# Kernel tuning notes

Hardware: AMD Instinct MI355X
Metric: run time of the kernel (lower is better)

## Reference

```python
import jax, jax.numpy as jnp
import numpy as np

EPS = 1e-5
ALPHA = 1.0

def _conv1x1(x, w, b):
    # x: [N,C,T,V], w: [O,C], b: [O] -> [N,O,T,V]
    return jnp.einsum('nctv,oc->notv', x, w) + b[None, :, None, None]

def _groupnorm1(x, gamma, beta):
    # GroupNorm(1, C): normalize over (C,T,V) per sample
    mu = jnp.mean(x, axis=(1, 2, 3), keepdims=True)
    var = jnp.var(x, axis=(1, 2, 3), keepdims=True)
    xn = (x - mu) * jax.lax.rsqrt(var + EPS)
    return xn * gamma[None, :, None, None] + beta[None, :, None, None]

def setup_inputs() -> dict:
    key = jax.random.key(0)
    ks = jax.random.split(key, 12)
    N, Cin, T, V, O, R = 128, 64, 128, 25, 64, 8
    s_in = 1.0 / np.sqrt(Cin)
    s_r = 1.0 / np.sqrt(R)
    return {
        'x':  jax.random.normal(ks[0], (N, Cin, T, V), jnp.float32),
        'A':  jax.random.normal(ks[1], (V, V), jnp.float32) * 0.1,
        'w1': jax.random.normal(ks[2], (R, Cin), jnp.float32) * s_in,
        'b1': jnp.zeros((R,), jnp.float32),
        'g1': jnp.ones((R,), jnp.float32),
        'be1': jnp.zeros((R,), jnp.float32),
        'w2': jax.random.normal(ks[3], (R, Cin), jnp.float32) * s_in,
        'b2': jnp.zeros((R,), jnp.float32),
        'g2': jnp.ones((R,), jnp.float32),
        'be2': jnp.zeros((R,), jnp.float32),
        'w3': jax.random.normal(ks[4], (O, Cin), jnp.float32) * s_in,
        'b3': jnp.zeros((O,), jnp.float32),
        'w4': jax.random.normal(ks[5], (O, R), jnp.float32) * s_r,
        'b4': jnp.zeros((O,), jnp.float32),
    }

def reference(x, A, w1, b1, g1, be1, w2, b2, g2, be2, w3, b3, w4, b4):
    # branch 1: conv1 -> GroupNorm -> temporal mean -> pairwise diff -> tanh
    x1 = _groupnorm1(_conv1x1(x, w1, b1), g1, be1).mean(axis=2)      # [N,R,V]
    y1 = jnp.tanh(x1[..., :, None] - x1[..., None, :])               # [N,R,V,V]
    # branch 2: conv2 -> GroupNorm -> temporal mean -> outer product -> tanh
    x2 = _groupnorm1(_conv1x1(x, w2, b2), g2, be2).mean(axis=2)      # [N,R,V]
    y2 = jnp.tanh(x2[..., :, None] * x2[..., None, :])               # [N,R,V,V]
    # value branch
    x3 = _conv1x1(x, w3, b3)                                          # [N,O,T,V]
    # dynamic adjacency: conv4 over rel channels
    ys = y1 + ALPHA * y2 + A[None, None]                              # [N,R,V,V]
    y_sum = jnp.einsum('nruv,or->nouv', ys, w4) + b4[None, :, None, None]
    # aggregation over vertices
    y = jnp.einsum('ncuv,nctv->nctu', y_sum, x3)                      # [N,O,T,V]
    return y
```

## Files before the change

### kernel.cpp

```cpp
#include <hip/hip_runtime.h>

#define EPSV 1e-5f
constexpr int NN = 128, CIN = 64, TT = 128, VV = 25, OO = 64, RR = 8;
constexpr int TVQ   = TT * VV;
constexpr int XSAMP = CIN * TVQ;
constexpr int YSAMP = OO * TT * VV;
constexpr int RTV   = RR * TT * VV;
constexpr int S12N  = 2 * RR * VV;
constexpr int YST_SAMP = VV * VV * OO;

__global__ __launch_bounds__(256) void kZero(float* __restrict__ p, int n)
{
    int i = blockIdx.x * 256 + threadIdx.x;
    if (i < n) p[i] = 0.f;
}

__global__ __launch_bounds__(256) void kA(const float* __restrict__ x,
    const float* __restrict__ w1, const float* __restrict__ b1,
    const float* __restrict__ w2, const float* __restrict__ b2,
    float* __restrict__ s12g, float* __restrict__ ssqg)
{
    __shared__ float wt1[CIN * RR], wt2[CIN * RR];
    __shared__ float s1l[RR * VV], s2l[RR * VV];
    __shared__ float redA[4], redB[4];
    const int tid = threadIdx.x;
    const int tc  = blockIdx.x;
    const int n   = blockIdx.y;

    for (int e = tid; e < CIN * RR; e += 256) {
        int r = e >> 6, c = e & 63;
        wt1[c * RR + r] = w1[e];
        wt2[c * RR + r] = w2[e];
    }
    for (int e = tid; e < 2 * RR * VV; e += 256) {
        if (e < RR * VV) s1l[e] = 0.f; else s2l[e - RR * VV] = 0.f;
    }
    __syncthreads();

    float acc1[4][RR], acc2[4][RR];
    #pragma unroll
    for (int j = 0; j < 4; ++j)
        #pragma unroll
        for (int r = 0; r < RR; ++r) { acc1[j][r] = 0.f; acc2[j][r] = 0.f; }

    const bool active = (tid < 200);
    const int p0 = tid * 4;
    const float* xb = x + (size_t)n * XSAMP + tc * 800 + p0;
    if (active) {
        #pragma unroll 4
        for (int c = 0; c < CIN; ++c) {
            float4 xv  = *(const float4*)(xb + c * TVQ);
            float4 wa1 = *(const float4*)(&wt1[c * RR]);
            float4 wb1 = *(const float4*)(&wt1[c * RR + 4]);
            float4 wa2 = *(const float4*)(&wt2[c * RR]);
            float4 wb2 = *(const float4*)(&wt2[c * RR + 4]);
            float xj[4]  = {xv.x, xv.y, xv.z, xv.w};
            float w1v[8] = {wa1.x, wa1.y, wa1.z, wa1.w, wb1.x, wb1.y, wb1.z, wb1.w};
            float w2v[8] = {wa2.x, wa2.y, wa2.z, wa2.w, wb2.x, wb2.y, wb2.z, wb2.w};
            #pragma unroll
            for (int j = 0; j < 4; ++j)
                #pragma unroll
                for (int r = 0; r < RR; ++r) {
                    acc1[j][r] += w1v[r] * xj[j];
                    acc2[j][r] += w2v[r] * xj[j];
                }
        }
    }

    float b1r[RR], b2r[RR];
    #pragma unroll
    for (int r = 0; r < RR; ++r) { b1r[r] = b1[r]; b2r[r] = b2[r]; }

    float ssq1 = 0.f, ssq2 = 0.f;
    if (active) {
        #pragma unroll
        for (int j = 0; j < 4; ++j) {
            int v = (p0 + j) % VV;
            #pragma unroll
            for (int r = 0; r < RR; ++r) {
                float c1 = acc1[j][r] + b1r[r]; ssq1 += c1 * c1;
                float c2 = acc2[j][r] + b2r[r]; ssq2 += c2 * c2;
                atomicAdd(&s1l[r * VV + v], acc1[j][r]);
                atomicAdd(&s2l[r * VV + v], acc2[j][r]);
            }
        }
    }
    #pragma unroll
    for (int off = 32; off > 0; off >>= 1) {
        ssq1 += __shfl_down(ssq1, off);
        ssq2 += __shfl_down(ssq2, off);
    }
    if ((tid & 63) == 0) { redA[tid >> 6] = ssq1; redB[tid >> 6] = ssq2; }
    __syncthreads();
    for (int e = tid; e < S12N; e += 256) {
        float pv = (e < RR * VV) ? s1l[e] : s2l[e - RR * VV];
        atomicAdd(&s12g[n * S12N + e], pv);
    }
    if (tid == 0) {
        atomicAdd(&ssqg[n * 2 + 0], redA[0] + redA[1] + redA[2] + redA[3]);
        atomicAdd(&ssqg[n * 2 + 1], redB[0] + redB[1] + redB[2] + redB[3]);
    }
}

__device__ __forceinline__ float tanh_fast(float v)
{
    float e = __expf(2.f * v);
    return 1.f - 2.f / (e + 1.f);
}

__global__ __launch_bounds__(512) void kB(
    const float* __restrict__ s12g, const float* __restrict__ ssqg,
    const float* __restrict__ b1, const float* __restrict__ g1, const float* __restrict__ be1,
    const float* __restrict__ b2, const float* __restrict__ g2, const float* __restrict__ be2,
    const float* __restrict__ Amat, const float* __restrict__ w4, const float* __restrict__ b4,
    float* __restrict__ ysumT)
{
    __shared__ float x1g[RR * VV], x2g[RR * VV];
    __shared__ float w4l[OO * RR];
    __shared__ float b4l[OO];
    __shared__ float stats[2];
    __shared__ float mss[4];
    const int tid = threadIdx.x;
    const int bx  = blockIdx.x;
    const int n   = blockIdx.y;

    if (tid < 2) stats[tid] = 0.f;
    if (tid < OO * RR) w4l[tid] = w4[tid];
    if (tid < OO) b4l[tid] = b4[tid];
    __syncthreads();

    float sv = 0.f;
    if (tid < S12N) {
        sv = s12g[n * S12N + tid];
        atomicAdd(&stats[tid / (RR * VV)], sv);
    }
    __syncthreads();
    if (tid == 0) {
        float sb1 = 0.f, sb2 = 0.f;
        for (int r = 0; r < RR; ++r) { sb1 += b1[r]; sb2 += b2[r]; }
        float mu1 = (stats[0] + (float)(TT * VV) * sb1) / (float)RTV;
        float mu2 = (stats[1] + (float)(TT * VV) * sb2) / (float)RTV;
        float var1 = ssqg[n * 2 + 0] / (float)RTV - mu1 * mu1;
        float var2 = ssqg[n * 2 + 1] / (float)RTV - mu2 * mu2;
        mss[0] = mu1; mss[1] = rsqrtf(var1 + EPSV);
        mss[2] = mu2; mss[3] = rsqrtf(var2 + EPSV);
    }
    __syncthreads();
    if (tid < S12N) {
        int br = tid / (RR * VV);
        int i  = tid % (RR * VV);
        int r  = i / VV;
        float mu = mss[br * 2], rs = mss[br * 2 + 1];
        float mean_t = sv / (float)TT + (br ? b2[r] : b1[r]);
        float g  = br ? g2[r]  : g1[r];
        float be = br ? be2[r] : be1[r];
        float val = g * (mean_t - mu) * rs + be;
        if (br == 0) x1g[i] = val; else x2g[i] = val;
    }
    __syncthreads();

    float* yn = ysumT + (size_t)n * YST_SAMP;
    const int pend = (bx + 1) * 125;
    for (int p = bx * 125 + tid; p < pend; p += 512) {
        int u = p / VV, v = p % VV;
        float Av = Amat[p];
        float ys[RR];
        #pragma unroll
        for (int r = 0; r < RR; ++r) {
            float d = x1g[r * VV + u] - x1g[r * VV + v];
            float m = x2g[r * VV + u] * x2g[r * VV + v];
            ys[r] = tanh_fast(d) + tanh_fast(m) + Av;
        }
        float* dst = yn + (size_t)p * OO;
        for (int o = 0; o < OO; ++o) {
            float a = b4l[o];
            #pragma unroll
            for (int r = 0; r < RR; ++r) a += w4l[o * RR + r] * ys[r];
            dst[o] = a;
        }
    }
}

__global__ __launch_bounds__(256) void kC(
    const float* __restrict__ x, const float* __restrict__ w3,
    const float* __restrict__ b3, const float* __restrict__ ysumT,
    float* __restrict__ y)
{
    __shared__ float lds[7168];
    const int tid = threadIdx.x;
    const int tc  = blockIdx.x;
    const int n   = blockIdx.y;
    const int t0  = tc * 8;

    const int og = tid >> 3;
    const int th = tid & 7;
    const int o0 = og * 2;

    float acc[2][VV];
    #pragma unroll
    for (int j = 0; j < 2; ++j)
        #pragma unroll
        for (int v = 0; v < VV; ++v) acc[j][v] = 0.f;

    const float* xn = x + (size_t)n * XSAMP + t0 * VV;
    #pragma unroll 1
    for (int cpass = 0; cpass < 2; ++cpass) {
        __syncthreads();
        for (int e4 = tid; e4 < 32 * 50; e4 += 256) {
            int cl = e4 / 50, r4 = (e4 % 50) * 4;
            float4 tv = *(const float4*)(xn + (cpass * 32 + cl) * TVQ + r4);
            float a[4] = {tv.x, tv.y, tv.z, tv.w};
            #pragma unroll
            for (int j = 0; j < 4; ++j) {
                int rem = r4 + j;
                lds[cl * 224 + (rem / VV) * 28 + (rem % VV)] = a[j];
            }
        }
        __syncthreads();
        #pragma unroll 1
        for (int q = 0; q < 2; ++q) {
            float w3q[2][16];
            #pragma unroll
            for (int j = 0; j < 2; ++j)
                #pragma unroll
                for (int k4 = 0; k4 < 4; ++k4) {
                    float4 wv = *(const float4*)(w3 + (o0 + j) * CIN
                                                 + cpass * 32 + q * 16 + k4 * 4);
                    w3q[j][k4*4+0] = wv.x; w3q[j][k4*4+1] = wv.y;
                    w3q[j][k4*4+2] = wv.z; w3q[j][k4*4+3] = wv.w;
                }
            #pragma unroll
            for (int ci = 0; ci < 16; ++ci) {
                const float* p = &lds[(q * 16 + ci) * 224 + th * 28];
                float4 a0 = *(const float4*)(p + 0);
                float4 a1 = *(const float4*)(p + 4);
                float4 a2 = *(const float4*)(p + 8);
                float4 a3 = *(const float4*)(p + 12);
                float4 a4 = *(const float4*)(p + 16);
                float4 a5 = *(const float4*)(p + 20);
                float  a6 = p[24];
                #pragma unroll
                for (int j = 0; j < 2; ++j) {
                    const float w = w3q[j][ci];
                    float* a = acc[j];
                    a[0]  += w*a0.x; a[1]  += w*a0.y; a[2]  += w*a0.z; a[3]  += w*a0.w;
                    a[4]  += w*a1.x; a[5]  += w*a1.y; a[6]  += w*a1.z; a[7]  += w*a1.w;
                    a[8]  += w*a2.x; a[9]  += w*a2.y; a[10] += w*a2.z; a[11] += w*a2.w;
                    a[12] += w*a3.x; a[13] += w*a3.y; a[14] += w*a3.z; a[15] += w*a3.w;
                    a[16] += w*a4.x; a[17] += w*a4.y; a[18] += w*a4.z; a[19] += w*a4.w;
                    a[20] += w*a5.x; a[21] += w*a5.y; a[22] += w*a5.z; a[23] += w*a5.w;
                    a[24] += w*a6;
                }
            }
        }
    }

    const int o2  = tid & 63;
    const int th2 = tid >> 6;
    const float bias = b3[o2];
    float acc2[2][VV];

    #pragma unroll 1
    for (int half = 0; half < 2; ++half) {
        __syncthreads();
        if ((th >> 2) == half) {
            const int tl = th & 3;
            #pragma unroll
            for (int j = 0; j < 2; ++j)
                #pragma unroll
                for (int v = 0; v < VV; ++v)
                    lds[tl * 1601 + (o0 + j) * VV + v] = acc[j][v];
        }
        __syncthreads();
        if ((th2 >> 1) == half) {
            #pragma unroll
            for (int row = 0; row < 2; ++row) {
                const int tl = (2 * th2 + row) & 3;
                #pragma unroll
                for (int v = 0; v < VV; ++v)
                    acc2[row][v] = lds[tl * 1601 + o2 * VV + v];
            }
        }
    }
    #pragma unroll
    for (int row = 0; row < 2; ++row)
        #pragma unroll
        for (int v = 0; v < VV; ++v) acc2[row][v] += bias;

    const float* yT = ysumT + (size_t)n * YST_SAMP + o2;
    float res[2][VV];
    #pragma unroll
    for (int u = 0; u < VV; ++u) {
        float r0 = 0.f, r1 = 0.f;
        #pragma unroll
        for (int v = 0; v < VV; ++v) {
            float yv = yT[(u * VV + v) * OO];
            r0 += yv * acc2[0][v];
            r1 += yv * acc2[1][v];
        }
        res[0][u] = r0;
        res[1][u] = r1;
    }

    float* yb = y + (size_t)n * YSAMP + t0 * VV;
    #pragma unroll 1
    for (int half = 0; half < 2; ++half) {
        __syncthreads();
        if ((th2 >> 1) == half) {
            #pragma unroll
            for (int row = 0; row < 2; ++row) {
                const int tl = (2 * th2 + row) & 3;
                #pragma unroll
                for (int u = 0; u < VV; ++u)
                    lds[o2 * 101 + tl * VV + u] = res[row][u];
            }
        }
        __syncthreads();
        for (int e = tid; e < 6400; e += 256) {
            int o = e / 100, m = e % 100;
            yb[o * TVQ + half * 100 + m] = lds[o * 101 + m];
        }
    }
}

extern "C" void kernel_launch(void* const* d_in, const int* in_sizes, int n_in,
                              void* d_out, int out_size, void* d_ws, size_t ws_size,
                              hipStream_t stream)
{
    const float* x   = (const float*)d_in[0];
    const float* Am  = (const float*)d_in[1];
    const float* w1  = (const float*)d_in[2];
    const float* b1  = (const float*)d_in[3];
    const float* g1  = (const float*)d_in[4];
    const float* be1 = (const float*)d_in[5];
    const float* w2  = (const float*)d_in[6];
    const float* b2  = (const float*)d_in[7];
    const float* g2  = (const float*)d_in[8];
    const float* be2 = (const float*)d_in[9];
    const float* w3  = (const float*)d_in[10];
    const float* b3  = (const float*)d_in[11];
    const float* w4  = (const float*)d_in[12];
    const float* b4  = (const float*)d_in[13];
    float* y  = (float*)d_out;
    float* ws = (float*)d_ws;
    float* s12g  = ws;
    float* ssqg  = ws + NN * S12N;
    float* ysumT = ws + NN * S12N + NN * 2;

    const int nz = NN * S12N + NN * 2;
    hipLaunchKernelGGL(kZero, dim3((nz + 255) / 256), dim3(256), 0, stream, ws, nz);
    hipLaunchKernelGGL(kA, dim3(4, NN), dim3(256), 0, stream,
                       x, w1, b1, w2, b2, s12g, ssqg);
    hipLaunchKernelGGL(kB, dim3(5, NN), dim3(512), 0, stream,
                       s12g, ssqg, b1, g1, be1, b2, g2, be2, Am, w4, b4, ysumT);
    hipLaunchKernelGGL(kC, dim3(16, NN), dim3(256), 0, stream,
                       x, w3, b3, ysumT, y);
}
```

Measured before the change: 444.8 us.

## Split value conv and vertex aggregation into separate kernels via workspace buffer

Replaces the fused kC kernel with two kernels. kC1 computes the 1x1 value convolution as a register-tiled 8x8 GEMM and writes x3 transposed to workspace. kC2 reads it back and does the per-sample vertex aggregation against ysumT. Work is chunked by how much workspace is available, and the old fused kernel is kept as a fallback. The split makes each stage simpler to tile but adds a full round-trip of the x3 intermediate (about 105 MB) through global memory.

Result: slower. 478.3 us (+7.5%).

```diff
diff --git a/kernel.cpp b/kernel.cpp
--- a/kernel.cpp
+++ b/kernel.cpp
@@ -8,6 +8,7 @@
 constexpr int RTV   = RR * TT * VV;
 constexpr int S12N  = 2 * RR * VV;
 constexpr int YST_SAMP = VV * VV * OO;
+constexpr int X3_SAMP  = TVQ * OO;
 
 __global__ __launch_bounds__(256) void kZero(float* __restrict__ p, int n)
 {
@@ -177,6 +178,125 @@
             #pragma unroll
             for (int r = 0; r < RR; ++r) a += w4l[o * RR + r] * ys[r];
             dst[o] = a;
+        }
+    }
+}
+
+__global__ __launch_bounds__(256) void kC1(const float* __restrict__ x,
+    const float* __restrict__ w3, const float* __restrict__ b3,
+    float* __restrict__ x3T)
+{
+    __shared__ float wt[CIN * 68];
+    const int tid = threadIdx.x;
+    const int n   = blockIdx.y;
+    const int oq  = tid & 7;
+    const int pg  = tid >> 3;
+    const int p0  = blockIdx.x * 256 + pg * 8;
+
+    for (int e = tid; e < CIN * OO; e += 256) {
+        int o = e >> 6, c = e & 63;
+        wt[c * 68 + o] = w3[e];
+    }
+    __syncthreads();
+
+    float acc[8][8];
+    #pragma unroll
+    for (int i = 0; i < 8; ++i)
+        #pragma unroll
+        for (int j = 0; j < 8; ++j) acc[i][j] = 0.f;
+
+    const bool act = (p0 < TVQ);
+    const float* xp = x + (size_t)n * XSAMP + p0;
+    if (act) {
+        #pragma unroll 4
+        for (int c = 0; c < CIN; ++c) {
+            const float* xc = xp + c * TVQ;
+            float4 xa = *(const float4*)(xc);
+            float4 xb = *(const float4*)(xc + 4);
+            const float* wr = &wt[c * 68 + oq * 8];
+            float4 wa = *(const float4*)(wr);
+            float4 wb = *(const float4*)(wr + 4);
+            float xv[8] = {xa.x, xa.y, xa.z, xa.w, xb.x, xb.y, xb.z, xb.w};
+            float wv[8] = {wa.x, wa.y, wa.z, wa.w, wb.x, wb.y, wb.z, wb.w};
+            #pragma unroll
+            for (int i = 0; i < 8; ++i)
+                #pragma unroll
+                for (int j = 0; j < 8; ++j)
+                    acc[i][j] += wv[i] * xv[j];
+        }
+    }
+
+    float bo[8];
+    #pragma unroll
+    for (int i = 0; i < 8; ++i) bo[i] = b3[oq * 8 + i];
+    if (act) {
+        float* dst = x3T + (size_t)n * X3_SAMP + (size_t)p0 * OO + oq * 8;
+        #pragma unroll
+        for (int j = 0; j < 8; ++j) {
+            float4 s0, s1;
+            s0.x = acc[0][j] + bo[0]; s0.y = acc[1][j] + bo[1];
+            s0.z = acc[2][j] + bo[2]; s0.w = acc[3][j] + bo[3];
+            s1.x = acc[4][j] + bo[4]; s1.y = acc[5][j] + bo[5];
+            s1.z = acc[6][j] + bo[6]; s1.w = acc[7][j] + bo[7];
+            *(float4*)(dst + j * OO)     = s0;
+            *(float4*)(dst + j * OO + 4) = s1;
+        }
+    }
+}
+
+__global__ __launch_bounds__(256) void kC2(const float* __restrict__ x3T,
+    const float* __restrict__ ysumT, float* __restrict__ y)
+{
+    __shared__ float lds[OO * 101];
+    const int tid = threadIdx.x;
+    const int tc  = blockIdx.x;
+    const int n   = blockIdx.y;
+    const int t0  = tc * 8;
+    const int o2  = tid & 63;
+    const int th2 = tid >> 6;
+
+    const float* xb = x3T + (size_t)n * X3_SAMP;
+    float acc2[2][VV];
+    #pragma unroll
+    for (int row = 0; row < 2; ++row) {
+        const int t = t0 + 2 * th2 + row;
+        #pragma unroll
+        for (int v = 0; v < VV; ++v)
+            acc2[row][v] = xb[(size_t)(t * VV + v) * OO + o2];
+    }
+
+    const float* yT = ysumT + (size_t)n * YST_SAMP + o2;
+    float res[2][VV];
+    #pragma unroll
+    for (int u = 0; u < VV; ++u) {
+        float r0 = 0.f, r1 = 0.f;
+        #pragma unroll
+        for (int v = 0; v < VV; ++v) {
+            float yv = yT[(u * VV + v) * OO];
+            r0 += yv * acc2[0][v];
+            r1 += yv * acc2[1][v];
+        }
+        res[0][u] = r0;
+        res[1][u] = r1;
+    }
+
+    float* yb = y + (size_t)n * YSAMP + t0 * VV;
+    #pragma unroll 1
+    for (int half = 0; half < 2; ++half) {
+        __syncthreads();
+        if ((th2 >> 1) == half) {
+            #pragma unroll
+            for (int row = 0; row < 2; ++row) {
+                const int tl = (2 * th2 + row) & 3;
+                #pragma unroll
+                for (int u = 0; u < VV; ++u)
+                    lds[o2 * 101 + tl * VV + u] = res[row][u];
+            }
+        }
+        __syncthreads();
+        for (int e = tid; e < 6400; e += 256) {
+            int o = e / 100, m = e % 100;
+            yb[o * TVQ + half * 100 + m] = lds[o * 101 + m];
         }
     }
 }
@@ -345,7 +465,8 @@
     float* ws = (float*)d_ws;
     float* s12g  = ws;
     float* ssqg  = ws + NN * S12N;
-    float* ysumT = ws + NN * S12N + NN * 2;
+    float* ysumT = ssqg + NN * 2;
+    float* x3T   = ysumT + (size_t)NN * YST_SAMP;
 
     const int nz = NN * S12N + NN * 2;
     hipLaunchKernelGGL(kZero, dim3((nz + 255) / 256), dim3(256), 0, stream, ws, nz);
@@ -353,6 +474,26 @@
                        x, w1, b1, w2, b2, s12g, ssqg);
     hipLaunchKernelGGL(kB, dim3(5, NN), dim3(512), 0, stream,
                        s12g, ssqg, b1, g1, be1, b2, g2, be2, Am, w4, b4, ysumT);
-    hipLaunchKernelGGL(kC, dim3(16, NN), dim3(256), 0, stream,
-                       x, w3, b3, ysumT, y);
-}
+
+    const size_t baseF = (size_t)NN * S12N + NN * 2 + (size_t)NN * YST_SAMP;
+    const size_t wsF   = ws_size / sizeof(float);
+    long availF = (long)wsF - (long)baseF;
+    int chunk = 0;
+    if (availF >= (long)X3_SAMP) {
+        long c = availF / (long)X3_SAMP;
+        chunk = (c > NN) ? NN : (int)c;
+    }
+    if (chunk >= 1) {
+        for (int n0 = 0; n0 < NN; n0 += chunk) {
+            int nc = (NN - n0 < chunk) ? (NN - n0) : chunk;
+            hipLaunchKernelGGL(kC1, dim3(13, nc), dim3(256), 0, stream,
+                               x + (size_t)n0 * XSAMP, w3, b3, x3T);
+            hipLaunchKernelGGL(kC2, dim3(16, nc), dim3(256), 0, stream,
+                               x3T, ysumT + (size_t)n0 * YST_SAMP,
+                               y + (size_t)n0 * YSAMP);
+        }
+    } else {
+        hipLaunchKernelGGL(kC, dim3(16, NN), dim3(256), 0, stream,
+                           x, w3, b3, ysumT, y);
+    }
+}
```
